# Optimization experiments

Measured on AMD Instinct MI355X. Metric: run time of the kernel, lower is better.

Reference implementation:

```python
import jax, jax.numpy as jnp
import numpy as np

N_RAYS = 8192
N_SAMPLES = 128
HIDDEN = 128
SH_DIM = 16
RAY_EXT_FACTOR = 10.0


def rsh_cart_3(d):
    # Real spherical harmonics up to degree 3, Cartesian form (16 coeffs).
    x, y, z = d[..., 0], d[..., 1], d[..., 2]
    x2, y2, z2 = x * x, y * y, z * z
    xy, yz, xz = x * y, y * z, x * z
    return jnp.stack([
        0.282094791773878 * jnp.ones_like(x),
        -0.48860251190292 * y,
        0.48860251190292 * z,
        -0.48860251190292 * x,
        1.0925484305920792 * xy,
        -1.0925484305920792 * yz,
        0.94617469575756 * z2 - 0.31539156525252,
        -1.0925484305920792 * xz,
        0.5462742152960396 * (x2 - y2),
        0.5900435899266435 * y * (-3.0 * x2 + y2),
        2.8906114426405538 * xy * z,
        0.4570457994644658 * y * (1.0 - 5.0 * z2),
        0.3731763325901154 * z * (5.0 * z2 - 3.0),
        0.4570457994644658 * x * (1.0 - 5.0 * z2),
        1.445305721320277 * z * (x2 - y2),
        0.5900435899266435 * x * (-x2 + 3.0 * y2),
    ], axis=-1)


def setup_inputs() -> dict:
    key = jax.random.key(0)
    ks = jax.random.split(key, 11)
    o = jax.random.normal(ks[0], (N_RAYS, 3), dtype=jnp.float32)
    origins = 2.5 * o / jnp.linalg.norm(o, axis=-1, keepdims=True)
    # aim roughly at the unit AABB so most rays are active
    dirs = -origins + 0.2 * jax.random.normal(ks[1], (N_RAYS, 3), dtype=jnp.float32)
    u = jax.random.uniform(ks[2], (N_RAYS, N_SAMPLES), dtype=jnp.float32)
    s1 = 1.0 / np.sqrt(3.0)
    s2 = 1.0 / np.sqrt(HIDDEN)
    s3 = 1.0 / np.sqrt(HIDDEN + SH_DIM)
    return {
        'origins': origins,
        'dirs': dirs,
        'u': u,
        'W1': s1 * jax.random.normal(ks[3], (3, HIDDEN), dtype=jnp.float32),
        'b1': jnp.zeros((HIDDEN,), jnp.float32),
        'W2': s2 * jax.random.normal(ks[4], (HIDDEN, HIDDEN), dtype=jnp.float32),
        'b2': jnp.zeros((HIDDEN,), jnp.float32),
        'Wd': s2 * jax.random.normal(ks[5], (HIDDEN, 1), dtype=jnp.float32),
        'bd': jnp.zeros((1,), jnp.float32),
        'Wc': s3 * jax.random.normal(ks[6], (HIDDEN + SH_DIM, 3), dtype=jnp.float32),
        'bc': jnp.zeros((3,), jnp.float32),
    }


def reference(origins, dirs, u, W1, b1, W2, b2, Wd, bd, Wc, bc):
    B, T = u.shape
    # ---- AABB ([-1,1]^3) slab intersection -> tnear/tfar, active mask ----
    inv_d = 1.0 / dirs
    t1 = (-1.0 - origins) * inv_d
    t2 = (1.0 - origins) * inv_d
    tnear = jnp.maximum(jnp.max(jnp.minimum(t1, t2), axis=-1), 0.0)  # (B,)
    tfar = jnp.min(jnp.maximum(t1, t2), axis=-1)                      # (B,)
    active = tfar > tnear                                             # (B,)
    tfar_c = jnp.maximum(tfar, tnear + 1e-3)
    # ---- stratified ray step sampling ----
    frac = (jnp.arange(T, dtype=u.dtype) + u) / T                     # (B,T)
    ts = tnear[:, None] + (tfar_c - tnear)[:, None] * frac            # (B,T)
    xyz = origins[:, None, :] + dirs[:, None, :] * ts[..., None]      # (B,T,3)
    # aabb is [-1,1]^3 so ndc == xyz; spatial filter = bounds test
    xyz_ndc = xyz
    mask = jnp.all(jnp.abs(xyz_ndc) <= 1.0, axis=-1) & active[:, None]  # (B,T)
    dnorm = jnp.linalg.norm(dirs, axis=-1)                            # (B,)
    ynm = rsh_cart_3(dirs / dnorm[:, None])                           # (B,16)
    # ---- radiance field MLP over all sample points ----
    x = xyz_ndc.reshape(B * T, 3)
    h = jax.nn.relu(x @ W1 + b1)
    h = jax.nn.relu(h @ W2 + b2)
    sigma = jax.nn.softplus(h @ Wd + bd).reshape(B, T)
    cond = jnp.broadcast_to(ynm[:, None, :], (B, T, SH_DIM)).reshape(B * T, SH_DIM)
    color = jax.nn.sigmoid(jnp.concatenate([h, cond], axis=-1) @ Wc + bc).reshape(B, T, 3)
    # zero out points rejected by the spatial filter (torch writes only masked)
    sigma = sigma * mask
    color = color * mask[..., None]
    # ---- transmittance integration (integrate_timesteps) ----
    tfinal = tfar_c * RAY_EXT_FACTOR
    deltas = jnp.diff(ts, axis=-1, append=tfinal[:, None])            # (B,T)
    sd = sigma * deltas * dnorm[:, None]
    csum = jnp.cumsum(sd, axis=-1)
    # weights_i = T_i * alpha_i = exp(-csum_{i-1}) - exp(-csum_i)
    weights = jnp.exp(sd - csum) - jnp.exp(-csum)                     # (B,T)
    color_out = jnp.einsum('bt,btc->bc', weights, color)              # (B,3)
    alpha_out = jnp.sum(weights, axis=-1, keepdims=True)              # (B,1)
    rgba = jnp.concatenate([color_out, alpha_out], axis=-1)           # (B,4)
    return jnp.where(active[:, None], rgba, 0.0)
```

## Files before the change

kernel.cpp:

```cpp
#include <hip/hip_runtime.h>
#include <math.h>

#define NRAYS 8192
#define T 128
#define H 128
#define SHD 16
#define RPB 2
#define NBLK (NRAYS / RPB)

using short8 = __attribute__((ext_vector_type(8))) short;
using f32x4  = __attribute__((ext_vector_type(4))) float;

__device__ __forceinline__ float softplus_f(float x) {
  return fmaxf(x, 0.f) + log1pf(expf(-fabsf(x)));
}

__device__ __forceinline__ unsigned f2bf(float f) {
  unsigned u = __float_as_uint(f);
  return (u + 0x7fffu + ((u >> 16) & 1u)) >> 16;
}

__global__ void preprocess(const float* __restrict__ W2, const float* __restrict__ Wd,
                           const float* __restrict__ Wc,
                           unsigned short* __restrict__ w2t,
                           unsigned short* __restrict__ woutf) {
  const int t = blockIdx.x * 256 + threadIdx.x;
  if (t < 16384) {
    const int n = t >> 7, p = t & 127;
    const int o = (p >> 3) ^ (n & 7);
    const int k = o * 8 + (p & 7);
    w2t[t] = (unsigned short)f2bf(W2[k * 128 + n]);
  }
  if (t < 2048) {
    const int kk = t >> 9, L = (t >> 3) & 63, j = t & 7;
    const int c = L & 15, g = L >> 4;
    const int k = kk * 32 + g * 8 + j;
    float v = 0.f;
    if (c == 0) v = Wd[k];
    else if (c < 4) v = Wc[k * 3 + (c - 1)];
    woutf[t] = (unsigned short)f2bf(v);
  }
}

__global__ __launch_bounds__(256, 2) void nerf_render(
    const float* __restrict__ origins, const float* __restrict__ dirs,
    const float* __restrict__ u, const float* __restrict__ W1,
    const float* __restrict__ b1, const float* __restrict__ b2,
    const float* __restrict__ bd, const float* __restrict__ Wc,
    const float* __restrict__ bc, const unsigned short* __restrict__ w2t,
    const unsigned short* __restrict__ woutf, float* __restrict__ out)
{
  const int ray0 = blockIdx.x * RPB;
  const int tid = threadIdx.x;
  const int L = tid & 63;
  const int w = tid >> 6;
  const int g = L >> 4;
  const int c = L & 15;

  __shared__ __align__(16) short Bs[16384];
  __shared__ __align__(16) short Wouts[2048];
  __shared__ __align__(16) short As2[4 * 640];
  __shared__ __align__(16) float4 xs4[RPB * T];
  __shared__ float mask_s[RPB * T];
  __shared__ __align__(16) float W1s[3 * H];
  __shared__ __align__(16) float b1s[H];
  __shared__ __align__(16) float b2s[H];
  __shared__ float sc_a[RPB * T], sc_b[RPB * T];
  __shared__ float wred[4][4];
  __shared__ float rayp[RPB][4];

  {
    const float4* src = (const float4*)w2t;
    float4* dst = (float4*)Bs;
    #pragma unroll
    for (int i = 0; i < 8; ++i) dst[tid + i * 256] = src[tid + i * 256];
    ((float4*)Wouts)[tid] = ((const float4*)woutf)[tid];
  }
  if (tid < H) { b1s[tid] = b1[tid]; b2s[tid] = b2[tid]; }
  for (int i = tid; i < 3 * H; i += 256) W1s[i] = W1[i];

  {
    const int r = tid >> 7, tl = tid & 127;
    const int gr = ray0 + r;
    const float ox = origins[gr*3+0], oy = origins[gr*3+1], oz = origins[gr*3+2];
    const float dx = dirs[gr*3+0],  dy = dirs[gr*3+1],  dz = dirs[gr*3+2];
    const float ix = 1.f/dx, iy = 1.f/dy, iz = 1.f/dz;
    const float t1x = (-1.f-ox)*ix, t2x = (1.f-ox)*ix;
    const float t1y = (-1.f-oy)*iy, t2y = (1.f-oy)*iy;
    const float t1z = (-1.f-oz)*iz, t2z = (1.f-oz)*iz;
    float tnear = fmaxf(fmaxf(fminf(t1x,t2x), fminf(t1y,t2y)), fminf(t1z,t2z));
    tnear = fmaxf(tnear, 0.f);
    const float tfar = fminf(fminf(fmaxf(t1x,t2x), fmaxf(t1y,t2y)), fmaxf(t1z,t2z));
    const bool  active = tfar > tnear;
    const float tfar_c = fmaxf(tfar, tnear + 1e-3f);
    const float ut = u[gr*T + tl];
    const float frac = ((float)tl + ut) * (1.f/(float)T);
    const float tt = tnear + (tfar_c - tnear) * frac;
    const float px = fmaf(dx, tt, ox);
    const float py = fmaf(dy, tt, oy);
    const float pz = fmaf(dz, tt, oz);
    xs4[tid] = make_float4(px, py, pz, tt);
    const bool m = (fabsf(px) <= 1.f) && (fabsf(py) <= 1.f) && (fabsf(pz) <= 1.f) && active;
    mask_s[tid] = m ? 1.f : 0.f;
    if (tl == 0) {
      rayp[r][0] = tfar_c;
      rayp[r][1] = sqrtf(dx*dx + dy*dy + dz*dz);
      rayp[r][2] = active ? 1.f : 0.f;
    }
  }
  __syncthreads();

  f32x4 acc[4][8];
  #pragma unroll
  for (int tm = 0; tm < 4; ++tm)
    #pragma unroll
    for (int mt = 0; mt < 8; ++mt)
      #pragma unroll
      for (int r = 0; r < 4; ++r) acc[tm][mt][r] = 0.f;

  const float4 xv0 = xs4[64*w + c];
  const float4 xv1 = xs4[64*w + 16 + c];
  const float4 xv2 = xs4[64*w + 32 + c];
  const float4 xv3 = xs4[64*w + 48 + c];

  #pragma unroll
  for (int ks = 0; ks < 4; ++ks) {
    const int kb = ks*32 + g*8;
    const float4 wxa = *(const float4*)&W1s[kb];
    const float4 wxb = *(const float4*)&W1s[kb+4];
    const float4 wya = *(const float4*)&W1s[128+kb];
    const float4 wyb = *(const float4*)&W1s[128+kb+4];
    const float4 wza = *(const float4*)&W1s[256+kb];
    const float4 wzb = *(const float4*)&W1s[256+kb+4];
    const float4 bba = *(const float4*)&b1s[kb];
    const float4 bbb = *(const float4*)&b1s[kb+4];
    const float wxv[8] = {wxa.x,wxa.y,wxa.z,wxa.w,wxb.x,wxb.y,wxb.z,wxb.w};
    const float wyv[8] = {wya.x,wya.y,wya.z,wya.w,wyb.x,wyb.y,wyb.z,wyb.w};
    const float wzv[8] = {wza.x,wza.y,wza.z,wza.w,wzb.x,wzb.y,wzb.z,wzb.w};
    const float bbv[8] = {bba.x,bba.y,bba.z,bba.w,bbb.x,bbb.y,bbb.z,bbb.w};
    short8 af0, af1, af2, af3;
    #pragma unroll
    for (int j = 0; j < 8; ++j) {
      const float wx = wxv[j], wy = wyv[j], wz = wzv[j], bb = bbv[j];
      const float v0 = fmaf(xv0.x, wx, fmaf(xv0.y, wy, fmaf(xv0.z, wz, bb)));
      const float v1 = fmaf(xv1.x, wx, fmaf(xv1.y, wy, fmaf(xv1.z, wz, bb)));
      const float v2 = fmaf(xv2.x, wx, fmaf(xv2.y, wy, fmaf(xv2.z, wz, bb)));
      const float v3 = fmaf(xv3.x, wx, fmaf(xv3.y, wy, fmaf(xv3.z, wz, bb)));
      af0[j] = (short)f2bf(fmaxf(v0, 0.f));
      af1[j] = (short)f2bf(fmaxf(v1, 0.f));
      af2[j] = (short)f2bf(fmaxf(v2, 0.f));
      af3[j] = (short)f2bf(fmaxf(v3, 0.f));
    }
    const int swb = ((ks*4 + g) ^ (c & 7)) * 8;
    #pragma unroll
    for (int mt = 0; mt < 8; ++mt) {
      const short8 wf = *(const short8*)&Bs[(mt*16 + c)*128 + swb];
      acc[0][mt] = __builtin_amdgcn_mfma_f32_16x16x32_bf16(wf, af0, acc[0][mt], 0, 0, 0);
      acc[1][mt] = __builtin_amdgcn_mfma_f32_16x16x32_bf16(wf, af1, acc[1][mt], 0, 0, 0);
      acc[2][mt] = __builtin_amdgcn_mfma_f32_16x16x32_bf16(wf, af2, acc[2][mt], 0, 0, 0);
      acc[3][mt] = __builtin_amdgcn_mfma_f32_16x16x32_bf16(wf, af3, acc[3][mt], 0, 0, 0);
    }
  }

  __syncthreads();
  float4* SredP = (float4*)Bs;

  short* As2w = As2 + w * 640;
  short8 wa[4];
  #pragma unroll
  for (int kk = 0; kk < 4; ++kk) wa[kk] = *(const short8*)&Wouts[(kk*64 + L)*8];

  #pragma unroll
  for (int tm = 0; tm < 4; ++tm) {
    f32x4 oacc;
    oacc[0] = 0.f; oacc[1] = 0.f; oacc[2] = 0.f; oacc[3] = 0.f;
    #pragma unroll
    for (int kk = 0; kk < 4; ++kk) {
      #pragma unroll
      for (int i = 0; i < 2; ++i) {
        const int mt = kk*2 + i;
        const float4 bv = *(const float4*)&b2s[mt*16 + g*4];
        const f32x4 a = acc[tm][mt];
        const float h0 = fmaxf(a[0] + bv.x, 0.f);
        const float h1 = fmaxf(a[1] + bv.y, 0.f);
        const float h2 = fmaxf(a[2] + bv.z, 0.f);
        const float h3 = fmaxf(a[3] + bv.w, 0.f);
        const unsigned p01 = f2bf(h0) | (f2bf(h1) << 16);
        const unsigned p23 = f2bf(h2) | (f2bf(h3) << 16);
        *(uint2*)&As2w[c*40 + i*16 + g*4] = make_uint2(p01, p23);
      }
      const short8 hb = *(const short8*)&As2w[c*40 + g*8];
      oacc = __builtin_amdgcn_mfma_f32_16x16x32_bf16(wa[kk], hb, oacc, 0, 0, 0);
    }
    if (g == 0)
      SredP[64*w + 16*tm + c] = make_float4(oacc[0], oacc[1], oacc[2], oacc[3]);
  }
  __syncthreads();

  const int r2 = tid >> 7, tl2 = tid & 127;
  const int gr2 = ray0 + r2;
  const float tfar_c2 = rayp[r2][0];
  const float dnorm2  = rayp[r2][1];
  const float4 sv = SredP[tid];
  const float mk = mask_s[tid];
  const float sigma = softplus_f(sv.x + bd[0]) * mk;
  float cc0, cc1, cc2;
  {
    const float dxr = dirs[gr2*3+0], dyr = dirs[gr2*3+1], dzr = dirs[gr2*3+2];
    const float nx = dxr/dnorm2, ny = dyr/dnorm2, nz = dzr/dnorm2;
    const float x2 = nx*nx, y2 = ny*ny, z2 = nz*nz;
    const float xy = nx*ny, yz = ny*nz, xz = nx*nz;
    float ynm[16];
    ynm[0]  = 0.282094791773878f;
    ynm[1]  = -0.48860251190292f*ny;
    ynm[2]  = 0.48860251190292f*nz;
    ynm[3]  = -0.48860251190292f*nx;
    ynm[4]  = 1.0925484305920792f*xy;
    ynm[5]  = -1.0925484305920792f*yz;
    ynm[6]  = 0.94617469575756f*z2 - 0.31539156525252f;
    ynm[7]  = -1.0925484305920792f*xz;
    ynm[8]  = 0.5462742152960396f*(x2-y2);
    ynm[9]  = 0.5900435899266435f*ny*(-3.f*x2+y2);
    ynm[10] = 2.8906114426405538f*xy*nz;
    ynm[11] = 0.4570457994644658f*ny*(1.f-5.f*z2);
    ynm[12] = 0.3731763325901154f*nz*(5.f*z2-3.f);
    ynm[13] = 0.4570457994644658f*nx*(1.f-5.f*z2);
    ynm[14] = 1.445305721320277f*nz*(x2-y2);
    ynm[15] = 0.5900435899266435f*nx*(-x2+3.f*y2);
    float cp0 = sv.y + bc[0], cp1 = sv.z + bc[1], cp2 = sv.w + bc[2];
    #pragma unroll
    for (int s = 0; s < SHD; ++s) {
      cp0 = fmaf(ynm[s], Wc[(H+s)*3+0], cp0);
      cp1 = fmaf(ynm[s], Wc[(H+s)*3+1], cp1);
      cp2 = fmaf(ynm[s], Wc[(H+s)*3+2], cp2);
    }
    cc0 = mk / (1.f + expf(-cp0));
    cc1 = mk / (1.f + expf(-cp1));
    cc2 = mk / (1.f + expf(-cp2));
  }
  const float tnext = (tl2 < T-1) ? xs4[tid+1].w : tfar_c2 * 10.f;
  const float sd = sigma * (tnext - xs4[tid].w) * dnorm2;
  sc_a[tid] = sd;
  __syncthreads();

  float* srcp = sc_a; float* dstp = sc_b;
  for (int off = 1; off < T; off <<= 1) {
    float v = srcp[tid];
    if (tl2 >= off) v += srcp[tid - off];
    __syncthreads();
    dstp[tid] = v;
    __syncthreads();
    float* tp = srcp; srcp = dstp; dstp = tp;
  }

  const float csum = srcp[tid];
  float wgt = expf(sd - csum) - expf(-csum);
  float wcx = wgt * cc0, wcy = wgt * cc1, wcz = wgt * cc2;
  #pragma unroll
  for (int mm = 32; mm >= 1; mm >>= 1) {
    wgt += __shfl_xor(wgt, mm);
    wcx += __shfl_xor(wcx, mm);
    wcy += __shfl_xor(wcy, mm);
    wcz += __shfl_xor(wcz, mm);
  }
  if (L == 0) { wred[w][0] = wgt; wred[w][1] = wcx; wred[w][2] = wcy; wred[w][3] = wcz; }
  __syncthreads();
  if (tid < RPB) {
    const int rr = tid;
    const float aw = wred[2*rr][0] + wred[2*rr+1][0];
    const float o0 = wred[2*rr][1] + wred[2*rr+1][1];
    const float o1 = wred[2*rr][2] + wred[2*rr+1][2];
    const float o2 = wred[2*rr][3] + wred[2*rr+1][3];
    const bool act = rayp[rr][2] != 0.f;
    out[(ray0+rr)*4+0] = act ? o0 : 0.f;
    out[(ray0+rr)*4+1] = act ? o1 : 0.f;
    out[(ray0+rr)*4+2] = act ? o2 : 0.f;
    out[(ray0+rr)*4+3] = act ? aw : 0.f;
  }
}

extern "C" void kernel_launch(void* const* d_in, const int* in_sizes, int n_in,
                              void* d_out, int out_size, void* d_ws, size_t ws_size,
                              hipStream_t stream) {
  const float* origins = (const float*)d_in[0];
  const float* dirs    = (const float*)d_in[1];
  const float* u       = (const float*)d_in[2];
  const float* W1      = (const float*)d_in[3];
  const float* b1      = (const float*)d_in[4];
  const float* W2      = (const float*)d_in[5];
  const float* b2      = (const float*)d_in[6];
  const float* Wd      = (const float*)d_in[7];
  const float* bd      = (const float*)d_in[8];
  const float* Wc      = (const float*)d_in[9];
  const float* bc      = (const float*)d_in[10];

  unsigned short* w2t   = (unsigned short*)d_ws;
  unsigned short* woutf = (unsigned short*)((char*)d_ws + 32768);

  preprocess<<<64, 256, 0, stream>>>(W2, Wd, Wc, w2t, woutf);
  nerf_render<<<NBLK, 256, 0, stream>>>(origins, dirs, u, W1, b1, b2, bd, Wc, bc,
                                        w2t, woutf, (float*)d_out);
}
```

Measured before the change: 161.2 us.

## Drop LDS weight staging, factor layer-1 per ray, use wave-shuffle scan

Rewrites layer 1 as a per-ray affine function of t (o·W1+b1 plus t·(d·W1)), so each sample needs one FMA per hidden unit. W2 and the output weights are no longer staged in shared memory and are read directly from global/L2 inside the MFMA loop. The b2 bias is folded into the accumulator initialisation, and the SH colour term is computed once per ray. A faster truncating bf16 pack is used, and the prefix scan becomes a wave shuffle scan instead of an LDS double-buffer with many barriers. Shared memory shrinks sharply, which could allow more occupancy, but the MFMA operands now depend on global-memory latency, and the rounding differs slightly (round-half-up, no ties-to-even).

```diff
diff --git a/kernel.cpp b/kernel.cpp
--- a/kernel.cpp
+++ b/kernel.cpp
@@ -20,15 +20,19 @@
   return (u + 0x7fffu + ((u >> 16) & 1u)) >> 16;
 }
 
+__device__ __forceinline__ unsigned pkbf(float a, float b) {
+  const unsigned ua = __float_as_uint(a) + 0x8000u;
+  const unsigned ub = __float_as_uint(b) + 0x8000u;
+  return __builtin_amdgcn_perm(ub, ua, 0x07060302u);
+}
+
 __global__ void preprocess(const float* __restrict__ W2, const float* __restrict__ Wd,
                            const float* __restrict__ Wc,
                            unsigned short* __restrict__ w2t,
                            unsigned short* __restrict__ woutf) {
   const int t = blockIdx.x * 256 + threadIdx.x;
   if (t < 16384) {
-    const int n = t >> 7, p = t & 127;
-    const int o = (p >> 3) ^ (n & 7);
-    const int k = o * 8 + (p & 7);
+    const int n = t >> 7, k = t & 127;
     w2t[t] = (unsigned short)f2bf(W2[k * 128 + n]);
   }
   if (t < 2048) {
@@ -57,27 +61,14 @@
   const int g = L >> 4;
   const int c = L & 15;
 
-  __shared__ __align__(16) short Bs[16384];
-  __shared__ __align__(16) short Wouts[2048];
+  __shared__ __align__(16) float2 bsl[RPB * H];
+  __shared__ float ts_s[RPB * T];
+  __shared__ float mask_s[RPB * T];
+  __shared__ __align__(16) float4 SredP[RPB * T];
   __shared__ __align__(16) short As2[4 * 640];
-  __shared__ __align__(16) float4 xs4[RPB * T];
-  __shared__ float mask_s[RPB * T];
-  __shared__ __align__(16) float W1s[3 * H];
-  __shared__ __align__(16) float b1s[H];
-  __shared__ __align__(16) float b2s[H];
-  __shared__ float sc_a[RPB * T], sc_b[RPB * T];
+  __shared__ float rayp[RPB][8];
   __shared__ float wred[4][4];
-  __shared__ float rayp[RPB][4];
-
-  {
-    const float4* src = (const float4*)w2t;
-    float4* dst = (float4*)Bs;
-    #pragma unroll
-    for (int i = 0; i < 8; ++i) dst[tid + i * 256] = src[tid + i * 256];
-    ((float4*)Wouts)[tid] = ((const float4*)woutf)[tid];
-  }
-  if (tid < H) { b1s[tid] = b1[tid]; b2s[tid] = b2[tid]; }
-  for (int i = tid; i < 3 * H; i += 256) W1s[i] = W1[i];
+  __shared__ float wtot[4];
 
   {
     const int r = tid >> 7, tl = tid & 127;
@@ -99,76 +90,100 @@
     const float px = fmaf(dx, tt, ox);
     const float py = fmaf(dy, tt, oy);
     const float pz = fmaf(dz, tt, oz);
-    xs4[tid] = make_float4(px, py, pz, tt);
+    ts_s[tid] = tt;
     const bool m = (fabsf(px) <= 1.f) && (fabsf(py) <= 1.f) && (fabsf(pz) <= 1.f) && active;
     mask_s[tid] = m ? 1.f : 0.f;
+    const float w0 = W1[tl], w1v = W1[H + tl], w2v = W1[2*H + tl];
+    bsl[r*H + tl] = make_float2(
+        fmaf(ox, w0, fmaf(oy, w1v, fmaf(oz, w2v, b1[tl]))),
+        fmaf(dx, w0, fmaf(dy, w1v, dz * w2v)));
     if (tl == 0) {
       rayp[r][0] = tfar_c;
-      rayp[r][1] = sqrtf(dx*dx + dy*dy + dz*dz);
+      const float dnorm = sqrtf(dx*dx + dy*dy + dz*dz);
+      rayp[r][1] = dnorm;
       rayp[r][2] = active ? 1.f : 0.f;
+      const float nx = dx/dnorm, ny = dy/dnorm, nz = dz/dnorm;
+      const float x2 = nx*nx, y2 = ny*ny, z2 = nz*nz;
+      const float xy = nx*ny, yz = ny*nz, xz = nx*nz;
+      float ynm[16];
+      ynm[0]  = 0.282094791773878f;
+      ynm[1]  = -0.48860251190292f*ny;
+      ynm[2]  = 0.48860251190292f*nz;
+      ynm[3]  = -0.48860251190292f*nx;
+      ynm[4]  = 1.0925484305920792f*xy;
+      ynm[5]  = -1.0925484305920792f*yz;
+      ynm[6]  = 0.94617469575756f*z2 - 0.31539156525252f;
+      ynm[7]  = -1.0925484305920792f*xz;
+      ynm[8]  = 0.5462742152960396f*(x2-y2);
+      ynm[9]  = 0.5900435899266435f*ny*(-3.f*x2+y2);
+      ynm[10] = 2.8906114426405538f*xy*nz;
+      ynm[11] = 0.4570457994644658f*ny*(1.f-5.f*z2);
+      ynm[12] = 0.3731763325901154f*nz*(5.f*z2-3.f);
+      ynm[13] = 0.4570457994644658f*nx*(1.f-5.f*z2);
+      ynm[14] = 1.445305721320277f*nz*(x2-y2);
+      ynm[15] = 0.5900435899266435f*nx*(-x2+3.f*y2);
+      float cp0 = bc[0], cp1 = bc[1], cp2 = bc[2];
+      #pragma unroll
+      for (int s = 0; s < SHD; ++s) {
+        cp0 = fmaf(ynm[s], Wc[(H+s)*3+0], cp0);
+        cp1 = fmaf(ynm[s], Wc[(H+s)*3+1], cp1);
+        cp2 = fmaf(ynm[s], Wc[(H+s)*3+2], cp2);
+      }
+      rayp[r][3] = cp0; rayp[r][4] = cp1; rayp[r][5] = cp2;
     }
   }
   __syncthreads();
 
   f32x4 acc[4][8];
   #pragma unroll
-  for (int tm = 0; tm < 4; ++tm)
-    #pragma unroll
-    for (int mt = 0; mt < 8; ++mt)
-      #pragma unroll
-      for (int r = 0; r < 4; ++r) acc[tm][mt][r] = 0.f;
-
-  const float4 xv0 = xs4[64*w + c];
-  const float4 xv1 = xs4[64*w + 16 + c];
-  const float4 xv2 = xs4[64*w + 32 + c];
-  const float4 xv3 = xs4[64*w + 48 + c];
+  for (int mt = 0; mt < 8; ++mt) {
+    const float4 bv = *(const float4*)&b2[mt*16 + g*4];
+    #pragma unroll
+    for (int tm = 0; tm < 4; ++tm) {
+      acc[tm][mt][0] = bv.x; acc[tm][mt][1] = bv.y;
+      acc[tm][mt][2] = bv.z; acc[tm][mt][3] = bv.w;
+    }
+  }
+
+  const int rayw = w >> 1;
+  const float t0 = ts_s[64*w + c];
+  const float t1 = ts_s[64*w + 16 + c];
+  const float t2 = ts_s[64*w + 32 + c];
+  const float t3 = ts_s[64*w + 48 + c];
+  const float2* bslr = bsl + rayw * H;
 
   #pragma unroll
   for (int ks = 0; ks < 4; ++ks) {
     const int kb = ks*32 + g*8;
-    const float4 wxa = *(const float4*)&W1s[kb];
-    const float4 wxb = *(const float4*)&W1s[kb+4];
-    const float4 wya = *(const float4*)&W1s[128+kb];
-    const float4 wyb = *(const float4*)&W1s[128+kb+4];
-    const float4 wza = *(const float4*)&W1s[256+kb];
-    const float4 wzb = *(const float4*)&W1s[256+kb+4];
-    const float4 bba = *(const float4*)&b1s[kb];
-    const float4 bbb = *(const float4*)&b1s[kb+4];
-    const float wxv[8] = {wxa.x,wxa.y,wxa.z,wxa.w,wxb.x,wxb.y,wxb.z,wxb.w};
-    const float wyv[8] = {wya.x,wya.y,wya.z,wya.w,wyb.x,wyb.y,wyb.z,wyb.w};
-    const float wzv[8] = {wza.x,wza.y,wza.z,wza.w,wzb.x,wzb.y,wzb.z,wzb.w};
-    const float bbv[8] = {bba.x,bba.y,bba.z,bba.w,bbb.x,bbb.y,bbb.z,bbb.w};
-    short8 af0, af1, af2, af3;
+    float ha[8], hb_[8], hc[8], hd[8];
     #pragma unroll
     for (int j = 0; j < 8; ++j) {
-      const float wx = wxv[j], wy = wyv[j], wz = wzv[j], bb = bbv[j];
-      const float v0 = fmaf(xv0.x, wx, fmaf(xv0.y, wy, fmaf(xv0.z, wz, bb)));
-      const float v1 = fmaf(xv1.x, wx, fmaf(xv1.y, wy, fmaf(xv1.z, wz, bb)));
-      const float v2 = fmaf(xv2.x, wx, fmaf(xv2.y, wy, fmaf(xv2.z, wz, bb)));
-      const float v3 = fmaf(xv3.x, wx, fmaf(xv3.y, wy, fmaf(xv3.z, wz, bb)));
-      af0[j] = (short)f2bf(fmaxf(v0, 0.f));
-      af1[j] = (short)f2bf(fmaxf(v1, 0.f));
-      af2[j] = (short)f2bf(fmaxf(v2, 0.f));
-      af3[j] = (short)f2bf(fmaxf(v3, 0.f));
-    }
-    const int swb = ((ks*4 + g) ^ (c & 7)) * 8;
+      const float2 p = bslr[kb + j];
+      ha[j]  = fmaxf(fmaf(t0, p.y, p.x), 0.f);
+      hb_[j] = fmaxf(fmaf(t1, p.y, p.x), 0.f);
+      hc[j]  = fmaxf(fmaf(t2, p.y, p.x), 0.f);
+      hd[j]  = fmaxf(fmaf(t3, p.y, p.x), 0.f);
+    }
+    union U { uint4 u; short8 s; } A0, A1, A2, A3;
+    A0.u = make_uint4(pkbf(ha[0],ha[1]),  pkbf(ha[2],ha[3]),  pkbf(ha[4],ha[5]),  pkbf(ha[6],ha[7]));
+    A1.u = make_uint4(pkbf(hb_[0],hb_[1]),pkbf(hb_[2],hb_[3]),pkbf(hb_[4],hb_[5]),pkbf(hb_[6],hb_[7]));
+    A2.u = make_uint4(pkbf(hc[0],hc[1]),  pkbf(hc[2],hc[3]),  pkbf(hc[4],hc[5]),  pkbf(hc[6],hc[7]));
+    A3.u = make_uint4(pkbf(hd[0],hd[1]),  pkbf(hd[2],hd[3]),  pkbf(hd[4],hd[5]),  pkbf(hd[6],hd[7]));
     #pragma unroll
     for (int mt = 0; mt < 8; ++mt) {
-      const short8 wf = *(const short8*)&Bs[(mt*16 + c)*128 + swb];
-      acc[0][mt] = __builtin_amdgcn_mfma_f32_16x16x32_bf16(wf, af0, acc[0][mt], 0, 0, 0);
-      acc[1][mt] = __builtin_amdgcn_mfma_f32_16x16x32_bf16(wf, af1, acc[1][mt], 0, 0, 0);
-      acc[2][mt] = __builtin_amdgcn_mfma_f32_16x16x32_bf16(wf, af2, acc[2][mt], 0, 0, 0);
-      acc[3][mt] = __builtin_amdgcn_mfma_f32_16x16x32_bf16(wf, af3, acc[3][mt], 0, 0, 0);
-    }
-  }
-
-  __syncthreads();
-  float4* SredP = (float4*)Bs;
+      const short8 wf = *(const short8*)&w2t[(mt*16 + c)*128 + kb];
+      acc[0][mt] = __builtin_amdgcn_mfma_f32_16x16x32_bf16(wf, A0.s, acc[0][mt], 0, 0, 0);
+      acc[1][mt] = __builtin_amdgcn_mfma_f32_16x16x32_bf16(wf, A1.s, acc[1][mt], 0, 0, 0);
+      acc[2][mt] = __builtin_amdgcn_mfma_f32_16x16x32_bf16(wf, A2.s, acc[2][mt], 0, 0, 0);
+      acc[3][mt] = __builtin_amdgcn_mfma_f32_16x16x32_bf16(wf, A3.s, acc[3][mt], 0, 0, 0);
+    }
+  }
 
   short* As2w = As2 + w * 640;
   short8 wa[4];
   #pragma unroll
-  for (int kk = 0; kk < 4; ++kk) wa[kk] = *(const short8*)&Wouts[(kk*64 + L)*8];
+  for (int kk = 0; kk < 4; ++kk)
+    wa[kk] = *(const short8*)&woutf[(kk*64 + L)*8];
 
   #pragma unroll
   for (int tm = 0; tm < 4; ++tm) {
@@ -178,19 +193,15 @@
     for (int kk = 0; kk < 4; ++kk) {
       #pragma unroll
       for (int i = 0; i < 2; ++i) {
-        const int mt = kk*2 + i;
-        const float4 bv = *(const float4*)&b2s[mt*16 + g*4];
-        const f32x4 a = acc[tm][mt];
-        const float h0 = fmaxf(a[0] + bv.x, 0.f);
-        const float h1 = fmaxf(a[1] + bv.y, 0.f);
-        const float h2 = fmaxf(a[2] + bv.z, 0.f);
-        const float h3 = fmaxf(a[3] + bv.w, 0.f);
-        const unsigned p01 = f2bf(h0) | (f2bf(h1) << 16);
-        const unsigned p23 = f2bf(h2) | (f2bf(h3) << 16);
-        *(uint2*)&As2w[c*40 + i*16 + g*4] = make_uint2(p01, p23);
+        const f32x4 a = acc[tm][kk*2 + i];
+        const float h0 = fmaxf(a[0], 0.f);
+        const float h1 = fmaxf(a[1], 0.f);
+        const float h2 = fmaxf(a[2], 0.f);
+        const float h3 = fmaxf(a[3], 0.f);
+        *(uint2*)&As2w[c*40 + i*16 + g*4] = make_uint2(pkbf(h0, h1), pkbf(h2, h3));
       }
-      const short8 hb = *(const short8*)&As2w[c*40 + g*8];
-      oacc = __builtin_amdgcn_mfma_f32_16x16x32_bf16(wa[kk], hb, oacc, 0, 0, 0);
+      const short8 hbf = *(const short8*)&As2w[c*40 + g*8];
+      oacc = __builtin_amdgcn_mfma_f32_16x16x32_bf16(wa[kk], hbf, oacc, 0, 0, 0);
     }
     if (g == 0)
       SredP[64*w + 16*tm + c] = make_float4(oacc[0], oacc[1], oacc[2], oacc[3]);
@@ -198,62 +209,31 @@
   __syncthreads();
 
   const int r2 = tid >> 7, tl2 = tid & 127;
-  const int gr2 = ray0 + r2;
   const float tfar_c2 = rayp[r2][0];
   const float dnorm2  = rayp[r2][1];
   const float4 sv = SredP[tid];
   const float mk = mask_s[tid];
   const float sigma = softplus_f(sv.x + bd[0]) * mk;
-  float cc0, cc1, cc2;
-  {
-    const float dxr = dirs[gr2*3+0], dyr = dirs[gr2*3+1], dzr = dirs[gr2*3+2];
-    const float nx = dxr/dnorm2, ny = dyr/dnorm2, nz = dzr/dnorm2;
-    const float x2 = nx*nx, y2 = ny*ny, z2 = nz*nz;
-    const float xy = nx*ny, yz = ny*nz, xz = nx*nz;
-    float ynm[16];
-    ynm[0]  = 0.282094791773878f;
-    ynm[1]  = -0.48860251190292f*ny;
-    ynm[2]  = 0.48860251190292f*nz;
-    ynm[3]  = -0.48860251190292f*nx;
-    ynm[4]  = 1.0925484305920792f*xy;
-    ynm[5]  = -1.0925484305920792f*yz;
-    ynm[6]  = 0.94617469575756f*z2 - 0.31539156525252f;
-    ynm[7]  = -1.0925484305920792f*xz;
-    ynm[8]  = 0.5462742152960396f*(x2-y2);
-    ynm[9]  = 0.5900435899266435f*ny*(-3.f*x2+y2);
-    ynm[10] = 2.8906114426405538f*xy*nz;
-    ynm[11] = 0.4570457994644658f*ny*(1.f-5.f*z2);
-    ynm[12] = 0.3731763325901154f*nz*(5.f*z2-3.f);
-    ynm[13] = 0.4570457994644658f*nx*(1.f-5.f*z2);
-    ynm[14] = 1.445305721320277f*nz*(x2-y2);
-    ynm[15] = 0.5900435899266435f*nx*(-x2+3.f*y2);
-    float cp0 = sv.y + bc[0], cp1 = sv.z + bc[1], cp2 = sv.w + bc[2];
-    #pragma unroll
-    for (int s = 0; s < SHD; ++s) {
-      cp0 = fmaf(ynm[s], Wc[(H+s)*3+0], cp0);
-      cp1 = fmaf(ynm[s], Wc[(H+s)*3+1], cp1);
-      cp2 = fmaf(ynm[s], Wc[(H+s)*3+2], cp2);
-    }
-    cc0 = mk / (1.f + expf(-cp0));
-    cc1 = mk / (1.f + expf(-cp1));
-    cc2 = mk / (1.f + expf(-cp2));
-  }
-  const float tnext = (tl2 < T-1) ? xs4[tid+1].w : tfar_c2 * 10.f;
-  const float sd = sigma * (tnext - xs4[tid].w) * dnorm2;
-  sc_a[tid] = sd;
-  __syncthreads();
-
-  float* srcp = sc_a; float* dstp = sc_b;
-  for (int off = 1; off < T; off <<= 1) {
-    float v = srcp[tid];
-    if (tl2 >= off) v += srcp[tid - off];
-    __syncthreads();
-    dstp[tid] = v;
-    __syncthreads();
-    float* tp = srcp; srcp = dstp; dstp = tp;
-  }
-
-  const float csum = srcp[tid];
+  const float cp0 = sv.y + rayp[r2][3];
+  const float cp1 = sv.z + rayp[r2][4];
+  const float cp2 = sv.w + rayp[r2][5];
+  const float cc0 = mk / (1.f + expf(-cp0));
+  const float cc1 = mk / (1.f + expf(-cp1));
+  const float cc2 = mk / (1.f + expf(-cp2));
+  const float tt = ts_s[tid];
+  const float tnext = (tl2 < T-1) ? ts_s[tid + 1] : tfar_c2 * 10.f;
+  const float sd = sigma * (tnext - tt) * dnorm2;
+
+  float val = sd;
+  #pragma unroll
+  for (int off = 1; off < 64; off <<= 1) {
+    const float tmp = __shfl_up(val, off);
+    if (L >= off) val += tmp;
+  }
+  if (L == 63) wtot[w] = val;
+  __syncthreads();
+  const float csum = val + ((w & 1) ? wtot[w - 1] : 0.f);
+
   float wgt = expf(sd - csum) - expf(-csum);
   float wcx = wgt * cc0, wcy = wgt * cc1, wcz = wgt * cc2;
   #pragma unroll
```

Result: slower. 172.6 us (+7.1%).
